# Performance work log

Measured on AMD Instinct MI355X. Metric: run time of the kernel, lower is better.

## Reference

```python
import jax, jax.numpy as jnp
import numpy as np

D_MODEL = 1024
N_HEAD = 16
B, T = 2, 2048

def setup_inputs() -> dict:
    key = jax.random.key(0)
    ks = jax.random.split(key, 6)
    s = 0.02
    return {
        "q_raw": jax.random.normal(ks[0], (B, T, D_MODEL), jnp.float32),
        "kv_raw": jax.random.normal(ks[1], (B, T, D_MODEL), jnp.float32),
        "kv_padding_mask": jnp.ones((B, T), jnp.int32),
        "Wq": jax.random.normal(ks[2], (D_MODEL, D_MODEL), jnp.float32) * s,
        "Wk": jax.random.normal(ks[3], (D_MODEL, D_MODEL), jnp.float32) * s,
        "Wv": jax.random.normal(ks[4], (D_MODEL, D_MODEL), jnp.float32) * s,
        "Wo": jax.random.normal(ks[5], (D_MODEL, D_MODEL), jnp.float32) * s,
    }

def reference(q_raw, kv_raw, kv_padding_mask, Wq, Wk, Wv, Wo):
    Bq, Tq, _ = q_raw.shape
    _, Tkv, _ = kv_raw.shape
    dh = D_MODEL // N_HEAD
    # projections (nn.Linear, no bias): x @ W.T
    q = (q_raw @ Wq.T).reshape(Bq, Tq, N_HEAD, dh).transpose(0, 2, 1, 3)   # (B,H,Tq,dh)
    k = (kv_raw @ Wk.T).reshape(Bq, Tkv, N_HEAD, dh).transpose(0, 2, 1, 3)  # (B,H,Tkv,dh)
    v = (kv_raw @ Wv.T).reshape(Bq, Tkv, N_HEAD, dh).transpose(0, 2, 1, 3)
    scores = jnp.einsum('bhqd,bhkd->bhqk', q, k) / jnp.sqrt(jnp.float32(dh))
    neg_inf = jnp.float32(-jnp.inf)
    # causal mask (is_causal_mask=True)
    causal = jnp.tril(jnp.ones((Tq, Tq), jnp.bool_))
    scores = jnp.where(causal[None, None, :, :], scores, neg_inf)
    # kv padding mask: (B,Tkv) -> (B,1,Tq,Tkv)
    pad = (kv_padding_mask != 0)[:, None, None, :]
    scores = jnp.where(pad, scores, neg_inf)
    weights = jax.nn.softmax(scores, axis=-1)
    y = jnp.einsum('bhqk,bhkd->bhqd', weights, v)   # (B,H,Tq,dh)
    # FAITHFUL to original: transpose(2,3) then view(B,Tq,-1)
    y = y.transpose(0, 1, 3, 2).reshape(Bq, Tq, -1)
    return y @ Wo.T
```

## Files before the change

kernel.cpp:

```cpp
#include <hip/hip_runtime.h>

#define B_SZ 2
#define T_SZ 2048
#define DM   1024
#define NH   16
#define DH   64

typedef __attribute__((ext_vector_type(8))) short bf16x8;
typedef __attribute__((ext_vector_type(4))) float f32x4;
typedef __attribute__((ext_vector_type(4))) unsigned int u32x4;
typedef __attribute__((ext_vector_type(4))) unsigned short u16x4;

__device__ __forceinline__ unsigned short f2bf(float f) {
  unsigned u = __builtin_bit_cast(unsigned, f);
  u += 0x7FFFu + ((u >> 16) & 1u);
  return (unsigned short)(u >> 16);
}
__device__ __forceinline__ unsigned packbf(float lo, float hi) {
  return (unsigned)f2bf(lo) | ((unsigned)f2bf(hi) << 16);
}

template<int CTRL>
__device__ __forceinline__ float dpp_mov(float x) {
  return __builtin_bit_cast(float,
      __builtin_amdgcn_update_dpp(0, __builtin_bit_cast(int, x), CTRL, 0xF, 0xF, true));
}
__device__ __forceinline__ float rowmax16(float x) {
  x = fmaxf(x, dpp_mov<0x128>(x));
  x = fmaxf(x, dpp_mov<0x124>(x));
  x = fmaxf(x, dpp_mov<0x122>(x));
  x = fmaxf(x, dpp_mov<0x121>(x));
  return x;
}
__device__ __forceinline__ float rowsum16(float x) {
  x += dpp_mov<0x128>(x);
  x += dpp_mov<0x124>(x);
  x += dpp_mov<0x122>(x);
  x += dpp_mov<0x121>(x);
  return x;
}

__device__ __forceinline__ void stage16(const float* src, unsigned short* dst) {
  const f32x4* ps = (const f32x4*)src;
  f32x4 v0 = ps[0], v1 = ps[1], v2 = ps[2], v3 = ps[3];
  u32x4 w0, w1;
  w0[0] = packbf(v0[0], v0[1]); w0[1] = packbf(v0[2], v0[3]);
  w0[2] = packbf(v1[0], v1[1]); w0[3] = packbf(v1[2], v1[3]);
  w1[0] = packbf(v2[0], v2[1]); w1[1] = packbf(v2[2], v2[3]);
  w1[2] = packbf(v3[0], v3[1]); w1[3] = packbf(v3[2], v3[3]);
  *(u32x4*)dst = w0;
  *(u32x4*)(dst + 8) = w1;
}

__device__ __forceinline__ void gload16(const unsigned short* g, unsigned short* l) {
  __builtin_amdgcn_global_load_lds(
      (const __attribute__((address_space(1))) unsigned int*)(const void*)g,
      (__attribute__((address_space(3))) unsigned int*)(void*)l, 16, 0, 0);
}

__device__ __forceinline__ void cvt16(const float* s, unsigned short* d, float scale) {
  const f32x4* ps = (const f32x4*)s;
  f32x4 v0 = ps[0] * scale, v1 = ps[1] * scale, v2 = ps[2] * scale, v3 = ps[3] * scale;
  u32x4 w0, w1;
  w0[0] = packbf(v0[0], v0[1]); w0[1] = packbf(v0[2], v0[3]);
  w0[2] = packbf(v1[0], v1[1]); w0[3] = packbf(v1[2], v1[3]);
  w1[0] = packbf(v2[0], v2[1]); w1[1] = packbf(v2[2], v2[3]);
  w1[2] = packbf(v3[0], v3[1]); w1[3] = packbf(v3[2], v3[3]);
  *(u32x4*)d = w0;
  *(u32x4*)(d + 8) = w1;
}

__global__ __launch_bounds__(256) void cvt_w4(
    const float* __restrict__ s0, const float* __restrict__ s1,
    const float* __restrict__ s2, const float* __restrict__ s3,
    unsigned short* __restrict__ d0, unsigned short* __restrict__ d1,
    unsigned short* __restrict__ d2, unsigned short* __restrict__ d3,
    float qscale) {
  const int y = blockIdx.y;
  const float* s = (y == 0) ? s0 : (y == 1) ? s1 : (y == 2) ? s2 : s3;
  unsigned short* d = (y == 0) ? d0 : (y == 1) ? d1 : (y == 2) ? d2 : d3;
  const float sc = (y == 0) ? qscale : 1.0f;
  const int i = (blockIdx.x * 256 + threadIdx.x) * 16;
  cvt16(s + i, d + i, sc);
}

__global__ __launch_bounds__(256) void cvt_in2(
    const float* __restrict__ s0, const float* __restrict__ s1,
    unsigned short* __restrict__ d0, unsigned short* __restrict__ d1) {
  const int y = blockIdx.y;
  const float* s = y ? s1 : s0;
  unsigned short* d = y ? d1 : d0;
  const int i = (blockIdx.x * 256 + threadIdx.x) * 16;
  cvt16(s + i, d + i, 1.0f);
}

template<int AMODE, int BMODE, int CMODE>
__global__ __launch_bounds__(256) void gemm2(
    const void* __restrict__ A0, const void* __restrict__ A1, int lda,
    const void* __restrict__ B0, const void* __restrict__ B1, int ldb, long bZ,
    void* __restrict__ C0, void* __restrict__ C1, int K, int nx, int ny) {
  __shared__ unsigned short As[128 * 32];
  __shared__ unsigned short Bs[64 * 32];
  const int tid = threadIdx.x, lane = tid & 63, w = tid >> 6;
  const int wm = w >> 1, wn = w & 1;
  const int l15 = lane & 15, lg = lane >> 4;

  const int cpx = gridDim.x >> 3;
  const int flat = (blockIdx.x & 7) * cpx + (blockIdx.x >> 3);
  const int nbk = flat % nx;
  const int rest = flat / nx;
  const int mbk = rest % ny;
  const int z = rest / ny;
  const int mblk = mbk * 128, nblk = nbk * 64;

  const void* Ap; const void* Bp; void* Cp;
  long aoff = 0; int zb = 0, zs = 0;
  if constexpr (CMODE == 0) {
    Ap = z ? A1 : A0; Bp = z ? B1 : B0; Cp = z ? C1 : C0;
  } else if constexpr (CMODE == 2) {
    Ap = A0; Cp = C0;
    if constexpr (BMODE == 1) Bp = (const void*)((const unsigned short*)B0 + (long)z * bZ);
    else                      Bp = (const void*)((const float*)B0 + (long)z * bZ);
  } else {
    Ap = A0; Bp = B0; Cp = C0;
    zb = z >> 1; zs = z & 1;
    aoff = (long)zb * 2097152 + (long)zs * 1024;
  }

  f32x4 acc[4][2];
#pragma unroll
  for (int i = 0; i < 4; i++)
#pragma unroll
    for (int j = 0; j < 2; j++) acc[i][j] = (f32x4){0.f, 0.f, 0.f, 0.f};

  const int asr = tid >> 1, asc = (tid & 1) * 16;
  const int agr = w * 32 + (lane >> 2), agc = (lane & 3) * 8;
  const int bgr = w * 16 + (lane >> 2), bgc = (lane & 3) * 8;

  for (int k0 = 0; k0 < K; k0 += 32) {
    if constexpr (AMODE == 0) {
      stage16((const float*)Ap + (long)(mblk + asr) * lda + k0 + asc, &As[asr * 32 + asc]);
    } else {
      const unsigned short* Ab = (const unsigned short*)Ap + aoff;
      gload16(Ab + (long)(mblk + agr) * lda + k0 + agc, &As[w * 1024]);
      gload16(Ab + (long)(mblk + agr + 16) * lda + k0 + agc, &As[w * 1024 + 512]);
    }
    if constexpr (BMODE == 0) {
      if (tid < 128)
        stage16((const float*)Bp + (long)(nblk + asr) * ldb + k0 + asc, &Bs[asr * 32 + asc]);
    } else {
      gload16((const unsigned short*)Bp + (long)(nblk + bgr) * ldb + k0 + bgc, &Bs[w * 512]);
    }
    __syncthreads();

    bf16x8 af[4], bfr[2];
#pragma unroll
    for (int mi = 0; mi < 4; mi++)
      af[mi] = *(const bf16x8*)&As[(wm * 64 + mi * 16 + l15) * 32 + lg * 8];
#pragma unroll
    for (int nj = 0; nj < 2; nj++)
      bfr[nj] = *(const bf16x8*)&Bs[(wn * 32 + nj * 16 + l15) * 32 + lg * 8];
#pragma unroll
    for (int mi = 0; mi < 4; mi++)
#pragma unroll
      for (int nj = 0; nj < 2; nj++)
        acc[mi][nj] = __builtin_amdgcn_mfma_f32_16x16x32_bf16(af[mi], bfr[nj], acc[mi][nj], 0, 0, 0);
    __syncthreads();
  }

#pragma unroll
  for (int mi = 0; mi < 4; mi++) {
#pragma unroll
    for (int nj = 0; nj < 2; nj++) {
#pragma unroll
      for (int r = 0; r < 4; r++) {
        const int i = mblk + wm * 64 + mi * 16 + lg * 4 + r;
        const int n = nblk + wn * 32 + nj * 16 + l15;
        const float v = acc[mi][nj][r];
        if constexpr (CMODE == 0) {
          const int b = i >> 11, t = i & 2047, h = n >> 6, d = n & 63;
          ((unsigned short*)Cp)[((long)(b * NH + h) * T_SZ + t) * DH + d] = f2bf(v);
        } else if constexpr (CMODE == 2) {
          ((unsigned short*)Cp)[(long)z * 2097152 + (long)i * 2048 + n] = f2bf(v);
        } else {
          ((float*)Cp)[(long)zb * T_SZ * DM + (long)(2 * i + zs) * DM + n] = v;
        }
      }
    }
  }
}

__global__ __launch_bounds__(512) void attn3(const unsigned short* __restrict__ Qh,
                                             const unsigned short* __restrict__ Kh,
                                             const unsigned short* __restrict__ Vt,
                                             const int* __restrict__ kmask,
                                             unsigned short* __restrict__ Zt) {
  __shared__ unsigned short lds_kv[2][2][64][72];
  __shared__ unsigned short lds_p[8][16][72];
  const int tid = threadIdx.x, lane = tid & 63, w = tid >> 6;
  const int l15 = lane & 15, lg = lane >> 4;
  const int g = w >> 2, sw = w & 3;
  const int wg = blockIdx.x;
  const int xcd = wg & 7, lin = wg >> 3;
  const int bh = xcd * 4 + (lin >> 4);
  const int p = lin & 15;
  const int b = bh >> 4, h = bh & 15;
  const int q0a = (31 - p) * 64;
  const int q0b = p * 64;
  const unsigned short* Qb = Qh + ((long)bh << 17);
  const unsigned short* Kb = Kh + ((long)bh << 17);
  const unsigned short* Vtb = Vt + ((long)(b * DM + h * DH)) * T_SZ;
  const long zbase = (long)(b * DM + h * DH) * T_SZ;

  int q0 = g ? q0b : q0a;
  bf16x8 qf0, qf1;
  {
    const int qra = q0 + sw * 16 + l15;
    qf0 = *(const bf16x8*)(Qb + ((long)qra << 6) + lg * 8);
    qf1 = *(const bf16x8*)(Qb + ((long)qra << 6) + 32 + lg * 8);
  }
  int qc0 = q0 + sw * 16 + lg * 4;

  f32x4 o[4];
  float mr[4], lr[4];
#pragma unroll
  for (int i = 0; i < 4; i++) {
    o[i] = (f32x4){0.f, 0.f, 0.f, 0.f};
    mr[i] = -1e30f; lr[i] = 0.f;
  }

  const int quarter = tid >> 7, sg = quarter >> 1, skv = quarter & 1;
  const int srow = (tid & 127) >> 1;
  const int soff = (tid & 1) * 32;
  const unsigned short* kp = Kb + ((long)srow << 6) + soff;
  const unsigned short* vp = Vtb + (long)srow * T_SZ + soff;

  u32x4 pr0, pr1, pr2, pr3;
  auto issue = [&](int it) {
    int j0s;
    if (sg == 0) j0s = it * 64;
    else j0s = (it <= p) ? it * 64 : ((it < 16) ? (16 + it - p) * 64 : 0);
    const u32x4* s = (const u32x4*)(skv ? (vp + j0s) : (kp + ((long)j0s << 6)));
    pr0 = s[0]; pr1 = s[1]; pr2 = s[2]; pr3 = s[3];
  };

  auto writeZ = [&](const f32x4* oo, const float* ll, int qq) {
    float inv[4];
#pragma unroll
    for (int r = 0; r < 4; r++) inv[r] = (ll[r] > 0.f) ? (1.f / ll[r]) : 0.f;
#pragma unroll
    for (int nb = 0; nb < 4; nb++) {
      u16x4 pk;
#pragma unroll
      for (int r = 0; r < 4; r++) pk[r] = f2bf(oo[nb][r] * inv[r]);
      *(u16x4*)&Zt[zbase + (long)(nb * 16 + l15) * T_SZ + qq] = pk;
    }
  };

  issue(0);
  for (int it = 0; it < 17; ++it) {
    __syncthreads();
    *(u32x4*)&lds_kv[sg][skv][srow][soff] = pr0;
    *(u32x4*)&lds_kv[sg][skv][srow][soff + 8] = pr1;
    *(u32x4*)&lds_kv[sg][skv][srow][soff + 16] = pr2;
    *(u32x4*)&lds_kv[sg][skv][srow][soff + 24] = pr3;
    __syncthreads();
    if (it + 1 < 17) issue(it + 1);

    if (g == 1 && it == p + 1) {
      writeZ(o, lr, qc0);
#pragma unroll
      for (int i = 0; i < 4; i++) {
        o[i] = (f32x4){0.f, 0.f, 0.f, 0.f};
        mr[i] = -1e30f; lr[i] = 0.f;
      }
      q0 = q0a;
      const int qra = q0 + sw * 16 + l15;
      qf0 = *(const bf16x8*)(Qb + ((long)qra << 6) + lg * 8);
      qf1 = *(const bf16x8*)(Qb + ((long)qra << 6) + 32 + lg * 8);
      qc0 = q0 + sw * 16 + lg * 4;
    }

    int j0 = it * 64;
    bool valid = true;
    if (g == 1) {
      if (it <= p) j0 = it * 64;
      else if (it < 16) j0 = (16 + it - p) * 64;
      else valid = false;
    }

    if (valid) {
      const int mk = kmask[b * T_SZ + j0 + lane];
      const unsigned long long kvm = __ballot(mk != 0);

      f32x4 sa[4];
      __builtin_amdgcn_s_setprio(1);
#pragma unroll
      for (int cb = 0; cb < 4; cb++) {
        bf16x8 kf0 = *(const bf16x8*)&lds_kv[g][0][cb * 16 + l15][lg * 8];
        bf16x8 kf1 = *(const bf16x8*)&lds_kv[g][0][cb * 16 + l15][32 + lg * 8];
        f32x4 t = {0.f, 0.f, 0.f, 0.f};
        t = __builtin_amdgcn_mfma_f32_16x16x32_bf16(qf0, kf0, t, 0, 0, 0);
        t = __builtin_amdgcn_mfma_f32_16x16x32_bf16(qf1, kf1, t, 0, 0, 0);
        sa[cb] = t;
      }
      __builtin_amdgcn_s_setprio(0);

      const bool diag = (j0 == q0);
      float tmax[4] = {-1e30f, -1e30f, -1e30f, -1e30f};
      if (!diag && kvm == ~0ull) {
#pragma unroll
        for (int cb = 0; cb < 4; cb++)
#pragma unroll
          for (int r = 0; r < 4; r++) tmax[r] = fmaxf(tmax[r], sa[cb][r]);
      } else {
#pragma unroll
        for (int cb = 0; cb < 4; cb++) {
          const int kk = cb * 16 + l15;
          const bool mk2 = (kvm >> kk) & 1ull;
#pragma unroll
          for (int r = 0; r < 4; r++) {
            float s = sa[cb][r];
            const bool ok = mk2 && (!diag || (j0 + kk <= qc0 + r));
            s = ok ? s : -1e30f;
            sa[cb][r] = s;
            tmax[r] = fmaxf(tmax[r], s);
          }
        }
      }
#pragma unroll
      for (int r = 0; r < 4; r++) {
        const float t = rowmax16(tmax[r]);
        const float mnew = fmaxf(mr[r], t);
        const float sc2 = __builtin_amdgcn_exp2f(mr[r] - mnew);
        mr[r] = mnew;
        float ts = 0.f;
#pragma unroll
        for (int cb = 0; cb < 4; cb++) {
          const float pe = __builtin_amdgcn_exp2f(sa[cb][r] - mnew);
          sa[cb][r] = pe;
          ts += pe;
        }
        ts = rowsum16(ts);
        lr[r] = lr[r] * sc2 + ts;
        o[0][r] *= sc2; o[1][r] *= sc2; o[2][r] *= sc2; o[3][r] *= sc2;
      }

#pragma unroll
      for (int cb = 0; cb < 4; cb++)
#pragma unroll
        for (int r = 0; r < 4; r++)
          lds_p[w][lg * 4 + r][cb * 16 + l15] = f2bf(sa[cb][r]);
      bf16x8 pf0 = *(const bf16x8*)&lds_p[w][l15][lg * 8];
      bf16x8 pf1 = *(const bf16x8*)&lds_p[w][l15][32 + lg * 8];

      __builtin_amdgcn_s_setprio(1);
#pragma unroll
      for (int nb = 0; nb < 4; nb++) {
        bf16x8 vf0 = *(const bf16x8*)&lds_kv[g][1][nb * 16 + l15][lg * 8];
        bf16x8 vf1 = *(const bf16x8*)&lds_kv[g][1][nb * 16 + l15][32 + lg * 8];
        f32x4 t = o[nb];
        t = __builtin_amdgcn_mfma_f32_16x16x32_bf16(pf0, vf0, t, 0, 0, 0);
        t = __builtin_amdgcn_mfma_f32_16x16x32_bf16(pf1, vf1, t, 0, 0, 0);
        o[nb] = t;
      }
      __builtin_amdgcn_s_setprio(0);
    }
  }

  __syncthreads();
  float* obuf = (float*)&lds_kv[0][0][0][0];
  float* mlb  = obuf + 4 * 16 * 65;
  if (g == 1) {
#pragma unroll
    for (int nb = 0; nb < 4; nb++)
#pragma unroll
      for (int r = 0; r < 4; r++)
        obuf[(sw * 16 + lg * 4 + r) * 65 + nb * 16 + l15] = o[nb][r];
    if (l15 == 0) {
#pragma unroll
      for (int r = 0; r < 4; r++) {
        mlb[(sw * 2 + 0) * 16 + lg * 4 + r] = mr[r];
        mlb[(sw * 2 + 1) * 16 + lg * 4 + r] = lr[r];
      }
    }
  }
  __syncthreads();
  if (g == 0) {
    float s0[4], s1[4], inv[4];
#pragma unroll
    for (int r = 0; r < 4; r++) {
      const float m1 = mlb[(sw * 2 + 0) * 16 + lg * 4 + r];
      const float l1 = mlb[(sw * 2 + 1) * 16 + lg * 4 + r];
      const float mm = fmaxf(mr[r], m1);
      s0[r] = __builtin_amdgcn_exp2f(mr[r] - mm);
      s1[r] = __builtin_amdgcn_exp2f(m1 - mm);
      const float ls = s0[r] * lr[r] + s1[r] * l1;
      inv[r] = (ls > 0.f) ? (1.f / ls) : 0.f;
    }
#pragma unroll
    for (int nb = 0; nb < 4; nb++) {
      u16x4 pk;
#pragma unroll
      for (int r = 0; r < 4; r++) {
        const float o1 = obuf[(sw * 16 + lg * 4 + r) * 65 + nb * 16 + l15];
        pk[r] = f2bf((s0[r] * o[nb][r] + s1[r] * o1) * inv[r]);
      }
      *(u16x4*)&Zt[zbase + (long)(nb * 16 + l15) * T_SZ + qc0] = pk;
    }
  }
}

extern "C" void kernel_launch(void* const* d_in, const int* in_sizes, int n_in,
                              void* d_out, int out_size, void* d_ws, size_t ws_size,
                              hipStream_t stream) {
  const float* q_raw  = (const float*)d_in[0];
  const float* kv_raw = (const float*)d_in[1];
  const int*   kmask  = (const int*)d_in[2];
  const float* Wq = (const float*)d_in[3];
  const float* Wk = (const float*)d_in[4];
  const float* Wv = (const float*)d_in[5];
  const float* Wo = (const float*)d_in[6];
  float* out = (float*)d_out;

  const float QSCALE = 0.125f * 1.44269504088896f;

  unsigned short* ws = (unsigned short*)d_ws;
  unsigned short* Qh = ws;
  unsigned short* Kh = ws + 4194304;
  unsigned short* Vt = ws + 8388608;
  unsigned short* Zt = ws + 12582912;
  const bool full = ws_size >= (size_t)58720256;

  if (full) {
    unsigned short* wqb = ws + 16777216;
    unsigned short* wkb = ws + 17825792;
    unsigned short* wvb = ws + 18874368;
    unsigned short* wob = ws + 19922944;
    unsigned short* qb  = ws + 20971520;
    unsigned short* kvb = ws + 25165824;
    cvt_w4<<<dim3(256, 4), 256, 0, stream>>>(Wq, Wk, Wv, Wo, wqb, wkb, wvb, wob, QSCALE);
    cvt_in2<<<dim3(1024, 2), 256, 0, stream>>>(q_raw, kv_raw, qb, kvb);
    gemm2<1, 1, 0><<<dim3(1024), 256, 0, stream>>>(
        qb, kvb, DM, wqb, wkb, DM, 0L, Qh, Kh, DM, 16, 32);
    gemm2<1, 1, 2><<<dim3(512), 256, 0, stream>>>(
        wvb, nullptr, DM, kvb, nullptr, DM, 2097152L, Vt, nullptr, DM, 32, 8);
    attn3<<<dim3(512), 512, 0, stream>>>(Qh, Kh, Vt, kmask, Zt);
    gemm2<1, 1, 1><<<dim3(512), 256, 0, stream>>>(
        Zt, nullptr, T_SZ, wob, nullptr, DM, 0L, out, nullptr, DM, 16, 8);
  } else {
    unsigned short* wqb = ws + 12582912;
    unsigned short* wkb = ws + 13631488;
    unsigned short* wvb = ws + 14680064;
    cvt_w4<<<dim3(256, 3), 256, 0, stream>>>(Wq, Wk, Wv, Wv, wqb, wkb, wvb, wvb, QSCALE);
    gemm2<0, 1, 0><<<dim3(1024), 256, 0, stream>>>(
        q_raw, kv_raw, DM, wqb, wkb, DM, 0L, Qh, Kh, DM, 16, 32);
    gemm2<1, 0, 2><<<dim3(512), 256, 0, stream>>>(
        wvb, nullptr, DM, kv_raw, nullptr, DM, 2097152L, Vt, nullptr, DM, 32, 8);
    attn3<<<dim3(512), 512, 0, stream>>>(Qh, Kh, Vt, kmask, Zt);
    gemm2<1, 0, 1><<<dim3(512), 256, 0, stream>>>(
        Zt, nullptr, T_SZ, Wo, nullptr, DM, 0L, out, nullptr, DM, 16, 8);
  }
}
```

Baseline: 138.0 us.

## Widen GEMM tiles to 128x128 and add lazy softmax rescaling in attention

The projection GEMMs now compute 128x128 output tiles per block instead of 128x64, doubling B-operand reuse and halving grid sizes. The attention kernel skips the running-max update and the rescaling of the accumulator and row sum when every lane's new block max exceeds the stored max by at most 8 (in log2 units). This reuses the stale max, bounding exponent growth at 2^8. Larger tiles raise accumulator register pressure and give fewer blocks for the 256 CUs, while lazy rescaling adds a wave-wide vote and branch.

```diff
diff --git a/kernel.cpp b/kernel.cpp
--- a/kernel.cpp
+++ b/kernel.cpp
@@ -95,12 +95,12 @@
 }
 
 template<int AMODE, int BMODE, int CMODE>
-__global__ __launch_bounds__(256) void gemm2(
+__global__ __launch_bounds__(256) void gemm3(
     const void* __restrict__ A0, const void* __restrict__ A1, int lda,
     const void* __restrict__ B0, const void* __restrict__ B1, int ldb, long bZ,
     void* __restrict__ C0, void* __restrict__ C1, int K, int nx, int ny) {
   __shared__ unsigned short As[128 * 32];
-  __shared__ unsigned short Bs[64 * 32];
+  __shared__ unsigned short Bs[128 * 32];
   const int tid = threadIdx.x, lane = tid & 63, w = tid >> 6;
   const int wm = w >> 1, wn = w & 1;
   const int l15 = lane & 15, lg = lane >> 4;
@@ -111,7 +111,7 @@
   const int rest = flat / nx;
   const int mbk = rest % ny;
   const int z = rest / ny;
-  const int mblk = mbk * 128, nblk = nbk * 64;
+  const int mblk = mbk * 128, nblk = nbk * 128;
 
   const void* Ap; const void* Bp; void* Cp;
   long aoff = 0; int zb = 0, zs = 0;
@@ -127,15 +127,14 @@
     aoff = (long)zb * 2097152 + (long)zs * 1024;
   }
 
-  f32x4 acc[4][2];
+  f32x4 acc[4][4];
 #pragma unroll
   for (int i = 0; i < 4; i++)
 #pragma unroll
-    for (int j = 0; j < 2; j++) acc[i][j] = (f32x4){0.f, 0.f, 0.f, 0.f};
+    for (int j = 0; j < 4; j++) acc[i][j] = (f32x4){0.f, 0.f, 0.f, 0.f};
 
   const int asr = tid >> 1, asc = (tid & 1) * 16;
   const int agr = w * 32 + (lane >> 2), agc = (lane & 3) * 8;
-  const int bgr = w * 16 + (lane >> 2), bgc = (lane & 3) * 8;
 
   for (int k0 = 0; k0 < K; k0 += 32) {
     if constexpr (AMODE == 0) {
@@ -146,24 +145,25 @@
       gload16(Ab + (long)(mblk + agr + 16) * lda + k0 + agc, &As[w * 1024 + 512]);
     }
     if constexpr (BMODE == 0) {
-      if (tid < 128)
-        stage16((const float*)Bp + (long)(nblk + asr) * ldb + k0 + asc, &Bs[asr * 32 + asc]);
+      stage16((const float*)Bp + (long)(nblk + asr) * ldb + k0 + asc, &Bs[asr * 32 + asc]);
     } else {
-      gload16((const unsigned short*)Bp + (long)(nblk + bgr) * ldb + k0 + bgc, &Bs[w * 512]);
+      const unsigned short* Bb = (const unsigned short*)Bp;
+      gload16(Bb + (long)(nblk + agr) * ldb + k0 + agc, &Bs[w * 1024]);
+      gload16(Bb + (long)(nblk + agr + 16) * ldb + k0 + agc, &Bs[w * 1024 + 512]);
     }
     __syncthreads();
 
-    bf16x8 af[4], bfr[2];
+    bf16x8 af[4], bfr[4];
 #pragma unroll
     for (int mi = 0; mi < 4; mi++)
       af[mi] = *(const bf16x8*)&As[(wm * 64 + mi * 16 + l15) * 32 + lg * 8];
 #pragma unroll
-    for (int nj = 0; nj < 2; nj++)
-      bfr[nj] = *(const bf16x8*)&Bs[(wn * 32 + nj * 16 + l15) * 32 + lg * 8];
+    for (int nj = 0; nj < 4; nj++)
+      bfr[nj] = *(const bf16x8*)&Bs[(wn * 64 + nj * 16 + l15) * 32 + lg * 8];
 #pragma unroll
     for (int mi = 0; mi < 4; mi++)
 #pragma unroll
-      for (int nj = 0; nj < 2; nj++)
+      for (int nj = 0; nj < 4; nj++)
         acc[mi][nj] = __builtin_amdgcn_mfma_f32_16x16x32_bf16(af[mi], bfr[nj], acc[mi][nj], 0, 0, 0);
     __syncthreads();
   }
@@ -171,11 +171,11 @@
 #pragma unroll
   for (int mi = 0; mi < 4; mi++) {
 #pragma unroll
-    for (int nj = 0; nj < 2; nj++) {
+    for (int nj = 0; nj < 4; nj++) {
 #pragma unroll
       for (int r = 0; r < 4; r++) {
         const int i = mblk + wm * 64 + mi * 16 + lg * 4 + r;
-        const int n = nblk + wn * 32 + nj * 16 + l15;
+        const int n = nblk + wn * 64 + nj * 16 + l15;
         const float v = acc[mi][nj][r];
         if constexpr (CMODE == 0) {
           const int b = i >> 11, t = i & 2047, h = n >> 6, d = n & 63;
@@ -328,22 +328,39 @@
           }
         }
       }
-#pragma unroll
-      for (int r = 0; r < 4; r++) {
-        const float t = rowmax16(tmax[r]);
-        const float mnew = fmaxf(mr[r], t);
-        const float sc2 = __builtin_amdgcn_exp2f(mr[r] - mnew);
-        mr[r] = mnew;
-        float ts = 0.f;
-#pragma unroll
-        for (int cb = 0; cb < 4; cb++) {
-          const float pe = __builtin_amdgcn_exp2f(sa[cb][r] - mnew);
-          sa[cb][r] = pe;
-          ts += pe;
+      float pm[4];
+#pragma unroll
+      for (int r = 0; r < 4; r++) pm[r] = rowmax16(tmax[r]);
+      const float need = fmaxf(fmaxf(pm[0] - mr[0], pm[1] - mr[1]),
+                               fmaxf(pm[2] - mr[2], pm[3] - mr[3]));
+      if (__all(need <= 8.0f)) {
+#pragma unroll
+        for (int r = 0; r < 4; r++) {
+          float ts = 0.f;
+#pragma unroll
+          for (int cb = 0; cb < 4; cb++) {
+            const float pe = __builtin_amdgcn_exp2f(sa[cb][r] - mr[r]);
+            sa[cb][r] = pe;
+            ts += pe;
+          }
+          lr[r] += rowsum16(ts);
         }
-        ts = rowsum16(ts);
-        lr[r] = lr[r] * sc2 + ts;
-        o[0][r] *= sc2; o[1][r] *= sc2; o[2][r] *= sc2; o[3][r] *= sc2;
+      } else {
+#pragma unroll
+        for (int r = 0; r < 4; r++) {
+          const float mnew = fmaxf(mr[r], pm[r]);
+          const float sc2 = __builtin_amdgcn_exp2f(mr[r] - mnew);
+          mr[r] = mnew;
+          float ts = 0.f;
+#pragma unroll
+          for (int cb = 0; cb < 4; cb++) {
+            const float pe = __builtin_amdgcn_exp2f(sa[cb][r] - mnew);
+            sa[cb][r] = pe;
+            ts += pe;
+          }
+          lr[r] = lr[r] * sc2 + rowsum16(ts);
+          o[0][r] *= sc2; o[1][r] *= sc2; o[2][r] *= sc2; o[3][r] *= sc2;
+        }
       }
 
 #pragma unroll
@@ -441,24 +458,24 @@
     unsigned short* kvb = ws + 25165824;
     cvt_w4<<<dim3(256, 4), 256, 0, stream>>>(Wq, Wk, Wv, Wo, wqb, wkb, wvb, wob, QSCALE);
     cvt_in2<<<dim3(1024, 2), 256, 0, stream>>>(q_raw, kv_raw, qb, kvb);
-    gemm2<1, 1, 0><<<dim3(1024), 256, 0, stream>>>(
-        qb, kvb, DM, wqb, wkb, DM, 0L, Qh, Kh, DM, 16, 32);
-    gemm2<1, 1, 2><<<dim3(512), 256, 0, stream>>>(
-        wvb, nullptr, DM, kvb, nullptr, DM, 2097152L, Vt, nullptr, DM, 32, 8);
+    gemm3<1, 1, 0><<<dim3(512), 256, 0, stream>>>(
+        qb, kvb, DM, wqb, wkb, DM, 0L, Qh, Kh, DM, 8, 32);
+    gemm3<1, 1, 2><<<dim3(256), 256, 0, stream>>>(
+        wvb, nullptr, DM, kvb, nullptr, DM, 2097152L, Vt, nullptr, DM, 16, 8);
     attn3<<<dim3(512), 512, 0, stream>>>(Qh, Kh, Vt, kmask, Zt);
-    gemm2<1, 1, 1><<<dim3(512), 256, 0, stream>>>(
-        Zt, nullptr, T_SZ, wob, nullptr, DM, 0L, out, nullptr, DM, 16, 8);
+    gemm3<1, 1, 1><<<dim3(256), 256, 0, stream>>>(
+        Zt, nullptr, T_SZ, wob, nullptr, DM, 0L, out, nullptr, DM, 8, 8);
   } else {
     unsigned short* wqb = ws + 12582912;
     unsigned short* wkb = ws + 13631488;
     unsigned short* wvb = ws + 14680064;
     cvt_w4<<<dim3(256, 3), 256, 0, stream>>>(Wq, Wk, Wv, Wv, wqb, wkb, wvb, wvb, QSCALE);
-    gemm2<0, 1, 0><<<dim3(1024), 256, 0, stream>>>(
-        q_raw, kv_raw, DM, wqb, wkb, DM, 0L, Qh, Kh, DM, 16, 32);
-    gemm2<1, 0, 2><<<dim3(512), 256, 0, stream>>>(
-        wvb, nullptr, DM, kv_raw, nullptr, DM, 2097152L, Vt, nullptr, DM, 32, 8);
+    gemm3<0, 1, 0><<<dim3(512), 256, 0, stream>>>(
+        q_raw, kv_raw, DM, wqb, wkb, DM, 0L, Qh, Kh, DM, 8, 32);
+    gemm3<1, 0, 2><<<dim3(256), 256, 0, stream>>>(
+        wvb, nullptr, DM, kv_raw, nullptr, DM, 2097152L, Vt, nullptr, DM, 16, 8);
     attn3<<<dim3(512), 512, 0, stream>>>(Qh, Kh, Vt, kmask, Zt);
-    gemm2<1, 0, 1><<<dim3(512), 256, 0, stream>>>(
-        Zt, nullptr, T_SZ, Wo, nullptr, DM, 0L, out, nullptr, DM, 16, 8);
-  }
-}
+    gemm3<1, 0, 1><<<dim3(256), 256, 0, stream>>>(
+        Zt, nullptr, T_SZ, Wo, nullptr, DM, 0L, out, nullptr, DM, 8, 8);
+  }
+}
```

After: 175.9 us. +27.5%, slower.
